# Kernel tuning notes

Hardware: AMD Instinct MI355X
Metric: run time of the kernel (lower is better)

The kernel has to match this reference:

```python
import jax, jax.numpy as jnp
import numpy as np

WIN = 8          # current_window
PRETRAIN = 8     # pretrain_window
HEADS = 8
SHIFT = WIN // 2 # shift_size, shift_dir = [1, 1] (shift_mode=1)
L = WIN * WIN
LOG100 = float(np.log(100.0))


def _shift_mask(H, W):
    # bands (shift_dir=[1,1], no padding). Pairs from different regions get -100.
    hr = np.repeat(np.arange(3), [H - WIN, WIN - SHIFT, SHIFT])
    wr = np.repeat(np.arange(3), [W - WIN, WIN - SHIFT, SHIFT])
    region = hr[:, None] * 3 + wr[None, :]                      # [H, W]
    reg = region.reshape(H // WIN, WIN, W // WIN, WIN)
    reg = reg.transpose(0, 2, 1, 3).reshape(-1, L)              # [nw, L]
    m = np.where(reg[:, :, None] != reg[:, None, :], -100.0, 0.0)
    return jnp.asarray(m, dtype=jnp.float32)[None, :, None]     # [1, nw, 1, L, L]


def _rel_bias(cpb_w1, cpb_b1, cpb_w2):
    # Swin-v2 continuous relative position bias (log-spaced coords + MLP).
    pos = np.stack(np.meshgrid(np.arange(WIN), np.arange(WIN), indexing='ij'), -1).reshape(L, 2)
    rc = (pos[:, None, :] - pos[None, :, :]).astype(np.float32)  # [L, L, 2]
    rc = rc / (PRETRAIN - 1) * 8.0
    rc = np.sign(rc) * np.log2(np.abs(rc) + 1.0) / np.log2(8.0)
    rc = jnp.asarray(rc)
    bias = jax.nn.relu(rc @ cpb_w1 + cpb_b1) @ cpb_w2            # [L, L, heads]
    bias = 16.0 * jax.nn.sigmoid(bias)
    return bias.transpose(2, 0, 1)                               # [heads, L, L]


def _l2n(a):
    # tf.math.l2_normalize with epsilon=1.55e-5
    return a * jax.lax.rsqrt(jnp.maximum(jnp.sum(a * a, -1, keepdims=True), 1.55e-5))


def setup_inputs() -> dict:
    key = jax.random.key(0)
    ks = jax.random.split(key, 6)
    B, H, W, C = 16, 128, 128, 256
    cpb = 512
    return {
        'x': jax.random.normal(ks[0], (B, H, W, C), jnp.float32),
        'qkv_w': jax.random.normal(ks[1], (C, 3 * C), jnp.float32) * 0.02,
        'q_bias': jnp.zeros((C,), jnp.float32),
        'v_bias': jnp.zeros((C,), jnp.float32),
        'scale': jnp.full((HEADS, 1, 1), np.log(10.0), jnp.float32),
        'cpb_w1': jax.random.normal(ks[2], (2, cpb), jnp.float32) * 0.02,
        'cpb_b1': jnp.zeros((cpb,), jnp.float32),
        'cpb_w2': jax.random.normal(ks[3], (cpb, HEADS), jnp.float32) * 0.02,
        'proj_w': jax.random.normal(ks[4], (C, C), jnp.float32) * 0.02,
        'proj_b': jnp.zeros((C,), jnp.float32),
    }


def reference(x, qkv_w, q_bias, v_bias, scale, cpb_w1, cpb_b1, cpb_w2, proj_w, proj_b):
    B, H, W, C = x.shape
    units = C // HEADS
    # qkv 1x1 conv + (q, 0, v) bias
    bias = jnp.concatenate([q_bias, jnp.zeros_like(q_bias), v_bias])
    qkv = jnp.einsum('bhwc,cd->bhwd', x, qkv_w) + bias
    # cyclic shift (H, W > window so shift is applied; no padding needed)
    qkv = jnp.roll(qkv, (-SHIFT, -SHIFT), axis=(1, 2))
    # fused window partition -> [B, nw, heads, L, 3*units]
    nh, nw = H // WIN, W // WIN
    t = qkv.reshape(B, nh, WIN, nw, WIN, HEADS, 3 * units)
    t = t.transpose(0, 1, 3, 5, 2, 4, 6).reshape(B, nh * nw, HEADS, L, 3 * units)
    q, k, v = jnp.split(t, 3, axis=-1)
    # cosine attention with clamped learned logit scale
    logit_scale = jnp.exp(jnp.minimum(scale, LOG100))            # [heads, 1, 1]
    attn = jnp.einsum('bnhld,bnhmd->bnhlm', _l2n(q) * logit_scale, _l2n(k))
    attn = attn + _rel_bias(cpb_w1, cpb_b1, cpb_w2)[None, None] + _shift_mask(H, W)
    attn = jax.nn.softmax(attn, axis=-1)
    out = jnp.einsum('bnhlm,bnhmd->bnhld', attn, v)
    # reverse partition, reverse shift, output projection
    out = out.reshape(B, nh, nw, HEADS, WIN, WIN, units)
    out = out.transpose(0, 1, 4, 2, 5, 3, 6).reshape(B, H, W, C)
    out = jnp.roll(out, (SHIFT, SHIFT), axis=(1, 2))
    return jnp.einsum('bhwc,cd->bhwd', out, proj_w) + proj_b
```

## Files before the change

kernel.cpp:

```cpp
#include <hip/hip_runtime.h>

typedef __attribute__((ext_vector_type(4))) float  f32x4;
typedef __attribute__((ext_vector_type(8))) __bf16 bf16x8;
typedef __attribute__((ext_vector_type(4))) __bf16 bf16x4;

__global__ __launch_bounds__(256) void wprep_kernel(const float* __restrict__ qw,
                                                    const float* __restrict__ pw,
                                                    const float* __restrict__ qb,
                                                    const float* __restrict__ vb,
                                                    __bf16* __restrict__ W2,
                                                    __bf16* __restrict__ Wp,
                                                    float* __restrict__ bcat) {
  int i = blockIdx.x * 256 + threadIdx.x;
  if (i < 24576) {
    int h = i / 3072, rem = i - h * 3072;
    int ft = rem >> 9, rem2 = rem & 511;
    int ks = rem2 >> 6, l = rem2 & 63;
    int g = l >> 4, c = l & 15;
    int col = h * 96 + ft * 16 + c;
    bf16x8 v;
    #pragma unroll
    for (int j = 0; j < 8; ++j)
      v[j] = (__bf16)qw[(ks * 32 + g * 8 + j) * 768 + col];
    *(bf16x8*)(W2 + (size_t)i * 8) = v;
  } else if (i < 24576 + 8192) {
    int j = i - 24576;
    int wv = j >> 10, rem = j & 1023;
    int ft = rem >> 9, rem2 = rem & 511;
    int ks = rem2 >> 6, l = rem2 & 63;
    int g = l >> 4, c = l & 15;
    int col = wv * 32 + ft * 16 + c;
    bf16x8 v;
    #pragma unroll
    for (int j8 = 0; j8 < 8; ++j8)
      v[j8] = (__bf16)pw[(ks * 32 + g * 8 + j8) * 256 + col];
    *(bf16x8*)(Wp + (size_t)j * 8) = v;
  } else if (i < 24576 + 8192 + 768) {
    int cdx = i - 24576 - 8192;
    bcat[cdx] = (cdx < 256) ? qb[cdx] : ((cdx < 512) ? 0.0f : vb[cdx - 512]);
  }
}

__global__ __launch_bounds__(256) void cpb_kernel(const float* __restrict__ w1,
                                                  const float* __restrict__ b1,
                                                  const float* __restrict__ w2,
                                                  float* __restrict__ bias) {
  int pair = blockIdx.x * 256 + threadIdx.x;
  int lq = pair >> 6, mk = pair & 63;
  float d0 = (float)((lq >> 3) - (mk >> 3));
  float d1 = (float)((lq & 7) - (mk & 7));
  float v0 = d0 * (8.0f / 7.0f);
  float v1 = d1 * (8.0f / 7.0f);
  float s0 = (v0 > 0.f) ? 1.f : ((v0 < 0.f) ? -1.f : 0.f);
  float s1 = (v1 > 0.f) ? 1.f : ((v1 < 0.f) ? -1.f : 0.f);
  float r0 = s0 * log2f(fabsf(v0) + 1.0f) * (1.0f / 3.0f);
  float r1 = s1 * log2f(fabsf(v1) + 1.0f) * (1.0f / 3.0f);
  float acc[8] = {0.f, 0.f, 0.f, 0.f, 0.f, 0.f, 0.f, 0.f};
  #pragma unroll 4
  for (int j = 0; j < 512; ++j) {
    float h = fmaxf(r0 * w1[j] + r1 * w1[512 + j] + b1[j], 0.0f);
    #pragma unroll
    for (int q = 0; q < 8; ++q) acc[q] += h * w2[j * 8 + q];
  }
  #pragma unroll
  for (int q = 0; q < 8; ++q) {
    float s = 16.0f / (1.0f + __expf(-acc[q]));
    bias[(q * 64 + lq) * 64 + mk] = s;
  }
}

__device__ __forceinline__ int win_region(int tok, int wi, int wj) {
  int r = tok >> 3, cc = tok & 7;
  int rh = (wi == 15) ? ((r < 4) ? 1 : 2) : 0;
  int rw = (wj == 15) ? ((cc < 4) ? 1 : 2) : 0;
  return rh * 3 + rw;
}

__global__ __launch_bounds__(512, 2) void fused_kernel(
    const float* __restrict__ x, const __bf16* __restrict__ W2,
    const __bf16* __restrict__ Wp, const float* __restrict__ bcat,
    const float* __restrict__ scale, const float* __restrict__ cpb,
    const float* __restrict__ pb, float* __restrict__ outf)
{
  __shared__ __align__(16) __bf16 xs[64 * 256];
  __shared__ __align__(16) __bf16 qkp[8][64 * 72];
  __shared__ __align__(16) __bf16 vst[8][64 * 36];
  const f32x4 zz = {0.f, 0.f, 0.f, 0.f};

  int t = threadIdx.x;
  int h = t >> 6, l = t & 63, g = l >> 4, c = l & 15;
  int win = blockIdx.x, b = blockIdx.y;
  int wi = win >> 4, wj = win & 15;
  bool edge = (wi == 15) || (wj == 15);

  {
    int r = t >> 3;
    int q8 = t & 7;
    int ht = (wi * 8 + (r >> 3) + 4) & 127;
    int wt = (wj * 8 + (r & 7) + 4) & 127;
    const float* src = x + (size_t)((b * 128 + ht) * 128 + wt) * 256 + q8 * 32;
    #pragma unroll
    for (int q = 0; q < 4; ++q) {
      f32x4 a0 = *(const f32x4*)(src + q * 8);
      f32x4 a1 = *(const f32x4*)(src + q * 8 + 4);
      bf16x8 v;
      #pragma unroll
      for (int j = 0; j < 4; ++j) { v[j] = (__bf16)a0[j]; v[4 + j] = (__bf16)a1[j]; }
      int phys = (q8 * 4 + q) ^ (r & 7);
      *(bf16x8*)&xs[r * 256 + phys * 8] = v;
    }
  }
  __syncthreads();

  int toko[4];
  #pragma unroll
  for (int i = 0; i < 4; ++i) {
    int tok = 16 * i + c;
    int ht = (wi * 8 + (tok >> 3) + 4) & 127;
    int wt = (wj * 8 + (tok & 7) + 4) & 127;
    toko[i] = ((b * 128 + ht) * 128 + wt) * 256;
  }

  f32x4 acc[6][4];
  #pragma unroll
  for (int ft = 0; ft < 6; ++ft)
    #pragma unroll
    for (int tt = 0; tt < 4; ++tt) acc[ft][tt] = zz;

  const __bf16* Wh = W2 + (size_t)h * 24576;
  #pragma unroll
  for (int ks = 0; ks < 8; ++ks) {
    bf16x8 wf[6], xf[4];
    #pragma unroll
    for (int ft = 0; ft < 6; ++ft)
      wf[ft] = *(const bf16x8*)(Wh + (size_t)((ft * 8 + ks) * 64 + l) * 8);
    #pragma unroll
    for (int tt = 0; tt < 4; ++tt) {
      int phys = (ks * 4 + g) ^ (c & 7);
      xf[tt] = *(const bf16x8*)&xs[(tt * 16 + c) * 256 + phys * 8];
    }
    #pragma unroll
    for (int ft = 0; ft < 6; ++ft)
      #pragma unroll
      for (int tt = 0; tt < 4; ++tt)
        acc[ft][tt] = __builtin_amdgcn_mfma_f32_16x16x32_bf16(wf[ft], xf[tt], acc[ft][tt], 0, 0, 0);
  }
  __syncthreads();

  #pragma unroll
  for (int ft = 0; ft < 6; ++ft) {
    f32x4 bb = *(const f32x4*)&bcat[h * 96 + ft * 16 + 4 * g];
    #pragma unroll
    for (int tt = 0; tt < 4; ++tt) acc[ft][tt] += bb;
  }

  float ls = __expf(fminf(scale[h], 4.6051701859880914f));

  #pragma unroll
  for (int tt = 0; tt < 4; ++tt) {
    float sq = 0.f, sk = 0.f;
    #pragma unroll
    for (int i = 0; i < 4; ++i) {
      sq += acc[0][tt][i] * acc[0][tt][i] + acc[1][tt][i] * acc[1][tt][i];
      sk += acc[2][tt][i] * acc[2][tt][i] + acc[3][tt][i] * acc[3][tt][i];
    }
    sq += __shfl_xor(sq, 16); sq += __shfl_xor(sq, 32);
    sk += __shfl_xor(sk, 16); sk += __shfl_xor(sk, 32);
    float rq = rsqrtf(fmaxf(sq, 1.55e-5f)) * ls;
    float rk = rsqrtf(fmaxf(sk, 1.55e-5f));
    __bf16* row = &qkp[h][(tt * 16 + c) * 72];
    bf16x4 w0, w1, w2, w3, v0, v1;
    #pragma unroll
    for (int i = 0; i < 4; ++i) {
      w0[i] = (__bf16)(acc[0][tt][i] * rq);
      w1[i] = (__bf16)(acc[1][tt][i] * rq);
      w2[i] = (__bf16)(acc[2][tt][i] * rk);
      w3[i] = (__bf16)(acc[3][tt][i] * rk);
      v0[i] = (__bf16)acc[4][tt][i];
      v1[i] = (__bf16)acc[5][tt][i];
    }
    *(bf16x4*)&row[4 * g]      = w0;
    *(bf16x4*)&row[16 + 4 * g] = w1;
    *(bf16x4*)&row[32 + 4 * g] = w2;
    *(bf16x4*)&row[48 + 4 * g] = w3;
    __bf16* vrow = &vst[h][(tt * 16 + c) * 36];
    *(bf16x4*)&vrow[4 * g]      = v0;
    *(bf16x4*)&vrow[16 + 4 * g] = v1;
  }

  bf16x8 kf[4], qf[4];
  #pragma unroll
  for (int i = 0; i < 4; ++i) {
    kf[i] = *(const bf16x8*)&qkp[h][(16 * i + c) * 72 + 32 + 8 * g];
    qf[i] = *(const bf16x8*)&qkp[h][(16 * i + c) * 72 + 8 * g];
  }

  float rsum[4];
  __bf16* Pw = &qkp[h][0];
  #pragma unroll
  for (int nt = 0; nt < 4; ++nt) {
    f32x4 tt4[4];
    #pragma unroll
    for (int mt = 0; mt < 4; ++mt)
      tt4[mt] = __builtin_amdgcn_mfma_f32_16x16x32_bf16(kf[mt], qf[nt], zz, 0, 0, 0);
    int q = nt * 16 + c;
    float p[16];
    #pragma unroll
    for (int mt = 0; mt < 4; ++mt) {
      f32x4 bb = *(const f32x4*)&cpb[(h * 64 + q) * 64 + mt * 16 + 4 * g];
      #pragma unroll
      for (int i = 0; i < 4; ++i) p[mt * 4 + i] = tt4[mt][i] + bb[i];
    }
    if (edge) {
      int regq = win_region(q, wi, wj);
      #pragma unroll
      for (int mt = 0; mt < 4; ++mt)
        #pragma unroll
        for (int i = 0; i < 4; ++i) {
          int k = mt * 16 + 4 * g + i;
          if (win_region(k, wi, wj) != regq) p[mt * 4 + i] -= 100.0f;
        }
    }
    float mx = -1e30f;
    #pragma unroll
    for (int j = 0; j < 16; ++j) mx = fmaxf(mx, p[j]);
    mx = fmaxf(mx, __shfl_xor(mx, 16));
    mx = fmaxf(mx, __shfl_xor(mx, 32));
    float sum = 0.f;
    #pragma unroll
    for (int j = 0; j < 16; ++j) { p[j] = __expf(p[j] - mx); sum += p[j]; }
    sum += __shfl_xor(sum, 16); sum += __shfl_xor(sum, 32);
    rsum[nt] = sum;
    #pragma unroll
    for (int mt = 0; mt < 4; ++mt) {
      bf16x4 px = { (__bf16)p[mt * 4 + 0], (__bf16)p[mt * 4 + 1],
                    (__bf16)p[mt * 4 + 2], (__bf16)p[mt * 4 + 3] };
      *(bf16x4*)&Pw[q * 72 + mt * 16 + 4 * g] = px;
    }
  }

  #pragma unroll
  for (int mh = 0; mh < 2; ++mh) {
    f32x4 oacc[4];
    #pragma unroll
    for (int nt = 0; nt < 4; ++nt) oacc[nt] = zz;
    #pragma unroll
    for (int ks = 0; ks < 2; ++ks) {
      bf16x8 va;
      #pragma unroll
      for (int j = 0; j < 8; ++j)
        va[j] = vst[h][(32 * ks + 8 * g + j) * 36 + 16 * mh + c];
      #pragma unroll
      for (int nt = 0; nt < 4; ++nt) {
        bf16x8 pfr = *(const bf16x8*)&Pw[(nt * 16 + c) * 72 + 32 * ks + 8 * g];
        oacc[nt] = __builtin_amdgcn_mfma_f32_16x16x32_bf16(va, pfr, oacc[nt], 0, 0, 0);
      }
    }
    int chunk = h * 4 + 2 * mh + (g >> 1);
    #pragma unroll
    for (int nt = 0; nt < 4; ++nt) {
      float rinv = 1.0f / rsum[nt];
      int tok = nt * 16 + c;
      int phys = chunk ^ (tok & 7);
      bf16x4 ov = { (__bf16)(oacc[nt][0] * rinv), (__bf16)(oacc[nt][1] * rinv),
                    (__bf16)(oacc[nt][2] * rinv), (__bf16)(oacc[nt][3] * rinv) };
      *(bf16x4*)&xs[tok * 256 + phys * 8 + 4 * (g & 1)] = ov;
    }
  }
  __syncthreads();

  f32x4 acc2[2][4];
  #pragma unroll
  for (int ft = 0; ft < 2; ++ft)
    #pragma unroll
    for (int tt = 0; tt < 4; ++tt) acc2[ft][tt] = zz;

  const __bf16* Wph = Wp + (size_t)h * 8192;
  #pragma unroll
  for (int ks = 0; ks < 8; ++ks) {
    bf16x8 wf[2], xf[4];
    #pragma unroll
    for (int ft = 0; ft < 2; ++ft)
      wf[ft] = *(const bf16x8*)(Wph + (size_t)((ft * 8 + ks) * 64 + l) * 8);
    #pragma unroll
    for (int tt = 0; tt < 4; ++tt) {
      int phys = (ks * 4 + g) ^ (c & 7);
      xf[tt] = *(const bf16x8*)&xs[(tt * 16 + c) * 256 + phys * 8];
    }
    #pragma unroll
    for (int ft = 0; ft < 2; ++ft)
      #pragma unroll
      for (int tt = 0; tt < 4; ++tt)
        acc2[ft][tt] = __builtin_amdgcn_mfma_f32_16x16x32_bf16(wf[ft], xf[tt], acc2[ft][tt], 0, 0, 0);
  }

  #pragma unroll
  for (int ft = 0; ft < 2; ++ft) {
    f32x4 bb = *(const f32x4*)&pb[h * 32 + ft * 16 + 4 * g];
    #pragma unroll
    for (int tt = 0; tt < 4; ++tt) {
      f32x4 res = acc2[ft][tt] + bb;
      *(f32x4*)&outf[toko[tt] + h * 32 + ft * 16 + 4 * g] = res;
    }
  }
}

extern "C" void kernel_launch(void* const* d_in, const int* in_sizes, int n_in,
                              void* d_out, int out_size, void* d_ws, size_t ws_size,
                              hipStream_t stream)
{
  const float* x      = (const float*)d_in[0];
  const float* qkv_w  = (const float*)d_in[1];
  const float* q_bias = (const float*)d_in[2];
  const float* v_bias = (const float*)d_in[3];
  const float* scale  = (const float*)d_in[4];
  const float* cpb_w1 = (const float*)d_in[5];
  const float* cpb_b1 = (const float*)d_in[6];
  const float* cpb_w2 = (const float*)d_in[7];
  const float* proj_w = (const float*)d_in[8];
  const float* proj_b = (const float*)d_in[9];

  char* ws = (char*)d_ws;
  __bf16* W2   = (__bf16*)(ws);
  __bf16* Wp   = (__bf16*)(ws + 393216LL);
  float*  bcat = (float*) (ws + 524288LL);
  float*  cpb  = (float*) (ws + 527360LL);

  wprep_kernel<<<131, 256, 0, stream>>>(qkv_w, proj_w, q_bias, v_bias, W2, Wp, bcat);
  cpb_kernel<<<16, 256, 0, stream>>>(cpb_w1, cpb_b1, cpb_w2, cpb);
  fused_kernel<<<dim3(256, 16), 512, 0, stream>>>(x, W2, Wp, bcat, scale, cpb,
                                                  proj_b, (float*)d_out);
}
```

Baseline: 430.4 us.

## Keep Q/K/P attention fragments in registers and drop qkp shared buffer

```diff
diff --git a/kernel.cpp b/kernel.cpp
--- a/kernel.cpp
+++ b/kernel.cpp
@@ -76,14 +76,13 @@
   return rh * 3 + rw;
 }
 
-__global__ __launch_bounds__(512, 2) void fused_kernel(
+__global__ __launch_bounds__(512, 4) void fused_kernel(
     const float* __restrict__ x, const __bf16* __restrict__ W2,
     const __bf16* __restrict__ Wp, const float* __restrict__ bcat,
     const float* __restrict__ scale, const float* __restrict__ cpb,
     const float* __restrict__ pb, float* __restrict__ outf)
 {
   __shared__ __align__(16) __bf16 xs[64 * 256];
-  __shared__ __align__(16) __bf16 qkp[8][64 * 72];
   __shared__ __align__(16) __bf16 vst[8][64 * 36];
   const f32x4 zz = {0.f, 0.f, 0.f, 0.f};
 
@@ -156,6 +155,7 @@
 
   float ls = __expf(fminf(scale[h], 4.6051701859880914f));
 
+  bf16x8 kA[4], qB[4];
   #pragma unroll
   for (int tt = 0; tt < 4; ++tt) {
     float sq = 0.f, sk = 0.f;
@@ -168,41 +168,44 @@
     sk += __shfl_xor(sk, 16); sk += __shfl_xor(sk, 32);
     float rq = rsqrtf(fmaxf(sq, 1.55e-5f)) * ls;
     float rk = rsqrtf(fmaxf(sk, 1.55e-5f));
-    __bf16* row = &qkp[h][(tt * 16 + c) * 72];
-    bf16x4 w0, w1, w2, w3, v0, v1;
+    bf16x4 v0, v1;
     #pragma unroll
     for (int i = 0; i < 4; ++i) {
-      w0[i] = (__bf16)(acc[0][tt][i] * rq);
-      w1[i] = (__bf16)(acc[1][tt][i] * rq);
-      w2[i] = (__bf16)(acc[2][tt][i] * rk);
-      w3[i] = (__bf16)(acc[3][tt][i] * rk);
+      qB[tt][i]     = (__bf16)(acc[0][tt][i] * rq);
+      qB[tt][4 + i] = (__bf16)(acc[1][tt][i] * rq);
+      kA[tt][i]     = (__bf16)(acc[2][tt][i] * rk);
+      kA[tt][4 + i] = (__bf16)(acc[3][tt][i] * rk);
       v0[i] = (__bf16)acc[4][tt][i];
       v1[i] = (__bf16)acc[5][tt][i];
     }
-    *(bf16x4*)&row[4 * g]      = w0;
-    *(bf16x4*)&row[16 + 4 * g] = w1;
-    *(bf16x4*)&row[32 + 4 * g] = w2;
-    *(bf16x4*)&row[48 + 4 * g] = w3;
     __bf16* vrow = &vst[h][(tt * 16 + c) * 36];
     *(bf16x4*)&vrow[4 * g]      = v0;
     *(bf16x4*)&vrow[16 + 4 * g] = v1;
   }
 
-  bf16x8 kf[4], qf[4];
-  #pragma unroll
-  for (int i = 0; i < 4; ++i) {
-    kf[i] = *(const bf16x8*)&qkp[h][(16 * i + c) * 72 + 32 + 8 * g];
-    qf[i] = *(const bf16x8*)&qkp[h][(16 * i + c) * 72 + 8 * g];
-  }
-
+  bf16x8 va[2][2];
+  #pragma unroll
+  for (int mh = 0; mh < 2; ++mh)
+    #pragma unroll
+    for (int kp = 0; kp < 2; ++kp)
+      #pragma unroll
+      for (int j = 0; j < 8; ++j)
+        va[mh][kp][j] =
+            vst[h][(32 * kp + 16 * (j >> 2) + 4 * g + (j & 3)) * 36 + 16 * mh + c];
+
+  f32x4 oacc[2][4];
+  #pragma unroll
+  for (int mh = 0; mh < 2; ++mh)
+    #pragma unroll
+    for (int nt = 0; nt < 4; ++nt) oacc[mh][nt] = zz;
   float rsum[4];
-  __bf16* Pw = &qkp[h][0];
+
   #pragma unroll
   for (int nt = 0; nt < 4; ++nt) {
     f32x4 tt4[4];
     #pragma unroll
     for (int mt = 0; mt < 4; ++mt)
-      tt4[mt] = __builtin_amdgcn_mfma_f32_16x16x32_bf16(kf[mt], qf[nt], zz, 0, 0, 0);
+      tt4[mt] = __builtin_amdgcn_mfma_f32_16x16x32_bf16(kA[mt], qB[nt], zz, 0, 0, 0);
     int q = nt * 16 + c;
     float p[16];
     #pragma unroll
@@ -231,39 +234,26 @@
     for (int j = 0; j < 16; ++j) { p[j] = __expf(p[j] - mx); sum += p[j]; }
     sum += __shfl_xor(sum, 16); sum += __shfl_xor(sum, 32);
     rsum[nt] = sum;
-    #pragma unroll
-    for (int mt = 0; mt < 4; ++mt) {
-      bf16x4 px = { (__bf16)p[mt * 4 + 0], (__bf16)p[mt * 4 + 1],
-                    (__bf16)p[mt * 4 + 2], (__bf16)p[mt * 4 + 3] };
-      *(bf16x4*)&Pw[q * 72 + mt * 16 + 4 * g] = px;
+    bf16x8 pf0, pf1;
+    #pragma unroll
+    for (int j = 0; j < 8; ++j) { pf0[j] = (__bf16)p[j]; pf1[j] = (__bf16)p[8 + j]; }
+    #pragma unroll
+    for (int mh = 0; mh < 2; ++mh) {
+      oacc[mh][nt] = __builtin_amdgcn_mfma_f32_16x16x32_bf16(va[mh][0], pf0, oacc[mh][nt], 0, 0, 0);
+      oacc[mh][nt] = __builtin_amdgcn_mfma_f32_16x16x32_bf16(va[mh][1], pf1, oacc[mh][nt], 0, 0, 0);
     }
   }
 
   #pragma unroll
   for (int mh = 0; mh < 2; ++mh) {
-    f32x4 oacc[4];
-    #pragma unroll
-    for (int nt = 0; nt < 4; ++nt) oacc[nt] = zz;
-    #pragma unroll
-    for (int ks = 0; ks < 2; ++ks) {
-      bf16x8 va;
-      #pragma unroll
-      for (int j = 0; j < 8; ++j)
-        va[j] = vst[h][(32 * ks + 8 * g + j) * 36 + 16 * mh + c];
-      #pragma unroll
-      for (int nt = 0; nt < 4; ++nt) {
-        bf16x8 pfr = *(const bf16x8*)&Pw[(nt * 16 + c) * 72 + 32 * ks + 8 * g];
-        oacc[nt] = __builtin_amdgcn_mfma_f32_16x16x32_bf16(va, pfr, oacc[nt], 0, 0, 0);
-      }
-    }
     int chunk = h * 4 + 2 * mh + (g >> 1);
     #pragma unroll
     for (int nt = 0; nt < 4; ++nt) {
       float rinv = 1.0f / rsum[nt];
       int tok = nt * 16 + c;
       int phys = chunk ^ (tok & 7);
-      bf16x4 ov = { (__bf16)(oacc[nt][0] * rinv), (__bf16)(oacc[nt][1] * rinv),
-                    (__bf16)(oacc[nt][2] * rinv), (__bf16)(oacc[nt][3] * rinv) };
+      bf16x4 ov = { (__bf16)(oacc[mh][nt][0] * rinv), (__bf16)(oacc[mh][nt][1] * rinv),
+                    (__bf16)(oacc[mh][nt][2] * rinv), (__bf16)(oacc[mh][nt][3] * rinv) };
       *(bf16x4*)&xs[tok * 256 + phys * 8 + 4 * (g & 1)] = ov;
     }
   }
```

Result: slower. 722.2 us (+67.8%).

## Split output projection into separate kernel via bf16 intermediate; merge prep kernels

Applied to the files above, without the earlier changes.

```diff
diff --git a/kernel.cpp b/kernel.cpp
--- a/kernel.cpp
+++ b/kernel.cpp
@@ -4,68 +4,66 @@
 typedef __attribute__((ext_vector_type(8))) __bf16 bf16x8;
 typedef __attribute__((ext_vector_type(4))) __bf16 bf16x4;
 
-__global__ __launch_bounds__(256) void wprep_kernel(const float* __restrict__ qw,
-                                                    const float* __restrict__ pw,
-                                                    const float* __restrict__ qb,
-                                                    const float* __restrict__ vb,
-                                                    __bf16* __restrict__ W2,
-                                                    __bf16* __restrict__ Wp,
-                                                    float* __restrict__ bcat) {
-  int i = blockIdx.x * 256 + threadIdx.x;
-  if (i < 24576) {
-    int h = i / 3072, rem = i - h * 3072;
-    int ft = rem >> 9, rem2 = rem & 511;
-    int ks = rem2 >> 6, l = rem2 & 63;
-    int g = l >> 4, c = l & 15;
-    int col = h * 96 + ft * 16 + c;
-    bf16x8 v;
-    #pragma unroll
-    for (int j = 0; j < 8; ++j)
-      v[j] = (__bf16)qw[(ks * 32 + g * 8 + j) * 768 + col];
-    *(bf16x8*)(W2 + (size_t)i * 8) = v;
-  } else if (i < 24576 + 8192) {
-    int j = i - 24576;
-    int wv = j >> 10, rem = j & 1023;
-    int ft = rem >> 9, rem2 = rem & 511;
-    int ks = rem2 >> 6, l = rem2 & 63;
-    int g = l >> 4, c = l & 15;
-    int col = wv * 32 + ft * 16 + c;
-    bf16x8 v;
-    #pragma unroll
-    for (int j8 = 0; j8 < 8; ++j8)
-      v[j8] = (__bf16)pw[(ks * 32 + g * 8 + j8) * 256 + col];
-    *(bf16x8*)(Wp + (size_t)j * 8) = v;
-  } else if (i < 24576 + 8192 + 768) {
-    int cdx = i - 24576 - 8192;
-    bcat[cdx] = (cdx < 256) ? qb[cdx] : ((cdx < 512) ? 0.0f : vb[cdx - 512]);
-  }
-}
-
-__global__ __launch_bounds__(256) void cpb_kernel(const float* __restrict__ w1,
-                                                  const float* __restrict__ b1,
-                                                  const float* __restrict__ w2,
-                                                  float* __restrict__ bias) {
-  int pair = blockIdx.x * 256 + threadIdx.x;
-  int lq = pair >> 6, mk = pair & 63;
-  float d0 = (float)((lq >> 3) - (mk >> 3));
-  float d1 = (float)((lq & 7) - (mk & 7));
-  float v0 = d0 * (8.0f / 7.0f);
-  float v1 = d1 * (8.0f / 7.0f);
-  float s0 = (v0 > 0.f) ? 1.f : ((v0 < 0.f) ? -1.f : 0.f);
-  float s1 = (v1 > 0.f) ? 1.f : ((v1 < 0.f) ? -1.f : 0.f);
-  float r0 = s0 * log2f(fabsf(v0) + 1.0f) * (1.0f / 3.0f);
-  float r1 = s1 * log2f(fabsf(v1) + 1.0f) * (1.0f / 3.0f);
-  float acc[8] = {0.f, 0.f, 0.f, 0.f, 0.f, 0.f, 0.f, 0.f};
-  #pragma unroll 4
-  for (int j = 0; j < 512; ++j) {
-    float h = fmaxf(r0 * w1[j] + r1 * w1[512 + j] + b1[j], 0.0f);
-    #pragma unroll
-    for (int q = 0; q < 8; ++q) acc[q] += h * w2[j * 8 + q];
-  }
-  #pragma unroll
-  for (int q = 0; q < 8; ++q) {
-    float s = 16.0f / (1.0f + __expf(-acc[q]));
-    bias[(q * 64 + lq) * 64 + mk] = s;
+__global__ __launch_bounds__(256) void prep_kernel(
+    const float* __restrict__ qw, const float* __restrict__ pw,
+    const float* __restrict__ qb, const float* __restrict__ vb,
+    const float* __restrict__ w1, const float* __restrict__ b1,
+    const float* __restrict__ w2,
+    __bf16* __restrict__ W2, __bf16* __restrict__ Wp,
+    float* __restrict__ bcat, float* __restrict__ cpbias)
+{
+  if (blockIdx.x < 131) {
+    int i = blockIdx.x * 256 + threadIdx.x;
+    if (i < 24576) {
+      int h = i / 3072, rem = i - h * 3072;
+      int ft = rem >> 9, rem2 = rem & 511;
+      int ks = rem2 >> 6, l = rem2 & 63;
+      int g = l >> 4, c = l & 15;
+      int col = h * 96 + ft * 16 + c;
+      bf16x8 v;
+      #pragma unroll
+      for (int j = 0; j < 8; ++j)
+        v[j] = (__bf16)qw[(ks * 32 + g * 8 + j) * 768 + col];
+      *(bf16x8*)(W2 + (size_t)i * 8) = v;
+    } else if (i < 24576 + 8192) {
+      int j = i - 24576;
+      int wv = j >> 10, rem = j & 1023;
+      int ft = rem >> 9, rem2 = rem & 511;
+      int ks = rem2 >> 6, l = rem2 & 63;
+      int g = l >> 4, c = l & 15;
+      int col = wv * 32 + ft * 16 + c;
+      bf16x8 v;
+      #pragma unroll
+      for (int j8 = 0; j8 < 8; ++j8)
+        v[j8] = (__bf16)pw[(ks * 32 + g * 8 + j8) * 256 + col];
+      *(bf16x8*)(Wp + (size_t)j * 8) = v;
+    } else if (i < 24576 + 8192 + 768) {
+      int cdx = i - 24576 - 8192;
+      bcat[cdx] = (cdx < 256) ? qb[cdx] : ((cdx < 512) ? 0.0f : vb[cdx - 512]);
+    }
+  } else {
+    int pair = (blockIdx.x - 131) * 256 + threadIdx.x;
+    int lq = pair >> 6, mk = pair & 63;
+    float d0 = (float)((lq >> 3) - (mk >> 3));
+    float d1 = (float)((lq & 7) - (mk & 7));
+    float v0 = d0 * (8.0f / 7.0f);
+    float v1 = d1 * (8.0f / 7.0f);
+    float s0 = (v0 > 0.f) ? 1.f : ((v0 < 0.f) ? -1.f : 0.f);
+    float s1 = (v1 > 0.f) ? 1.f : ((v1 < 0.f) ? -1.f : 0.f);
+    float r0 = s0 * log2f(fabsf(v0) + 1.0f) * (1.0f / 3.0f);
+    float r1 = s1 * log2f(fabsf(v1) + 1.0f) * (1.0f / 3.0f);
+    float acc[8] = {0.f, 0.f, 0.f, 0.f, 0.f, 0.f, 0.f, 0.f};
+    #pragma unroll 4
+    for (int j = 0; j < 512; ++j) {
+      float h = fmaxf(r0 * w1[j] + r1 * w1[512 + j] + b1[j], 0.0f);
+      #pragma unroll
+      for (int q = 0; q < 8; ++q) acc[q] += h * w2[j * 8 + q];
+    }
+    #pragma unroll
+    for (int q = 0; q < 8; ++q) {
+      float s = 16.0f / (1.0f + __expf(-acc[q]));
+      cpbias[(q * 64 + lq) * 64 + mk] = s;
+    }
   }
 }
 
@@ -78,9 +76,8 @@
 
 __global__ __launch_bounds__(512, 2) void fused_kernel(
     const float* __restrict__ x, const __bf16* __restrict__ W2,
-    const __bf16* __restrict__ Wp, const float* __restrict__ bcat,
-    const float* __restrict__ scale, const float* __restrict__ cpb,
-    const float* __restrict__ pb, float* __restrict__ outf)
+    const float* __restrict__ bcat, const float* __restrict__ scale,
+    const float* __restrict__ cpb, __bf16* __restrict__ out)
 {
   __shared__ __align__(16) __bf16 xs[64 * 256];
   __shared__ __align__(16) __bf16 qkp[8][64 * 72];
@@ -145,7 +142,6 @@
       for (int tt = 0; tt < 4; ++tt)
         acc[ft][tt] = __builtin_amdgcn_mfma_f32_16x16x32_bf16(wf[ft], xf[tt], acc[ft][tt], 0, 0, 0);
   }
-  __syncthreads();
 
   #pragma unroll
   for (int ft = 0; ft < 6; ++ft) {
@@ -256,51 +252,66 @@
         oacc[nt] = __builtin_amdgcn_mfma_f32_16x16x32_bf16(va, pfr, oacc[nt], 0, 0, 0);
       }
     }
-    int chunk = h * 4 + 2 * mh + (g >> 1);
     #pragma unroll
     for (int nt = 0; nt < 4; ++nt) {
       float rinv = 1.0f / rsum[nt];
-      int tok = nt * 16 + c;
-      int phys = chunk ^ (tok & 7);
       bf16x4 ov = { (__bf16)(oacc[nt][0] * rinv), (__bf16)(oacc[nt][1] * rinv),
                     (__bf16)(oacc[nt][2] * rinv), (__bf16)(oacc[nt][3] * rinv) };
-      *(bf16x4*)&xs[tok * 256 + phys * 8 + 4 * (g & 1)] = ov;
+      *(bf16x4*)(out + toko[nt] + h * 32 + 16 * mh + 4 * g) = ov;
+    }
+  }
+}
+
+__global__ __launch_bounds__(512, 4) void proj2_kernel(
+    const __bf16* __restrict__ A, const __bf16* __restrict__ Wp,
+    const float* __restrict__ pb, float* __restrict__ outf)
+{
+  __shared__ __align__(16) __bf16 os[128 * 256];
+  const f32x4 zz = {0.f, 0.f, 0.f, 0.f};
+  int t = threadIdx.x;
+  int wv = t >> 6, l = t & 63, g = l >> 4, c = l & 15;
+  int mblk = blockIdx.x;
+
+  {
+    int r = t >> 2;
+    int q4 = t & 3;
+    const __bf16* src = A + (size_t)(mblk * 128 + r) * 256 + q4 * 64;
+    #pragma unroll
+    for (int q = 0; q < 8; ++q) {
+      bf16x8 v = *(const bf16x8*)(src + q * 8);
+      int phys = (q4 * 8 + q) ^ (r & 7);
+      *(bf16x8*)&os[r * 256 + phys * 8] = v;
     }
   }
   __syncthreads();
 
-  f32x4 acc2[2][4];
+  f32x4 acc[2][8];
   #pragma unroll
   for (int ft = 0; ft < 2; ++ft)
     #pragma unroll
-    for (int tt = 0; tt < 4; ++tt) acc2[ft][tt] = zz;
-
-  const __bf16* Wph = Wp + (size_t)h * 8192;
+    for (int tt = 0; tt < 8; ++tt) acc[ft][tt] = zz;
+
+  const __bf16* Wph = Wp + (size_t)wv * 8192;
   #pragma unroll
   for (int ks = 0; ks < 8; ++ks) {
-    bf16x8 wf[2], xf[4];
-    #pragma unroll
-    for (int ft = 0; ft < 2; ++ft)
-      wf[ft] = *(const bf16x8*)(Wph + (size_t)((ft * 8 + ks) * 64 + l) * 8);
-    #pragma unroll
-    for (int tt = 0; tt < 4; ++tt) {
+    bf16x8 w0 = *(const bf16x8*)(Wph + (size_t)((0 * 8 + ks) * 64 + l) * 8);
+    bf16x8 w1 = *(const bf16x8*)(Wph + (size_t)((1 * 8 + ks) * 64 + l) * 8);
+    #pragma unroll
+    for (int tt = 0; tt < 8; ++tt) {
       int phys = (ks * 4 + g) ^ (c & 7);
-      xf[tt] = *(const bf16x8*)&xs[(tt * 16 + c) * 256 + phys * 8];
-    }
-    #pragma unroll
-    for (int ft = 0; ft < 2; ++ft)
-      #pragma unroll
-      for (int tt = 0; tt < 4; ++tt)
-        acc2[ft][tt] = __builtin_amdgcn_mfma_f32_16x16x32_bf16(wf[ft], xf[tt], acc2[ft][tt], 0, 0, 0);
+      bf16x8 xf = *(const bf16x8*)&os[(tt * 16 + c) * 256 + phys * 8];
+      acc[0][tt] = __builtin_amdgcn_mfma_f32_16x16x32_bf16(w0, xf, acc[0][tt], 0, 0, 0);
+      acc[1][tt] = __builtin_amdgcn_mfma_f32_16x16x32_bf16(w1, xf, acc[1][tt], 0, 0, 0);
+    }
   }
 
   #pragma unroll
   for (int ft = 0; ft < 2; ++ft) {
-    f32x4 bb = *(const f32x4*)&pb[h * 32 + ft * 16 + 4 * g];
-    #pragma unroll
-    for (int tt = 0; tt < 4; ++tt) {
-      f32x4 res = acc2[ft][tt] + bb;
-      *(f32x4*)&outf[toko[tt] + h * 32 + ft * 16 + 4 * g] = res;
+    f32x4 bb = *(const f32x4*)&pb[wv * 32 + ft * 16 + 4 * g];
+    #pragma unroll
+    for (int tt = 0; tt < 8; ++tt) {
+      f32x4 res = acc[ft][tt] + bb;
+      *(f32x4*)&outf[(size_t)(mblk * 128 + tt * 16 + c) * 256 + wv * 32 + ft * 16 + 4 * g] = res;
     }
   }
 }
@@ -321,13 +332,14 @@
   const float* proj_b = (const float*)d_in[9];
 
   char* ws = (char*)d_ws;
-  __bf16* W2   = (__bf16*)(ws);
-  __bf16* Wp   = (__bf16*)(ws + 393216LL);
-  float*  bcat = (float*) (ws + 524288LL);
-  float*  cpb  = (float*) (ws + 527360LL);
-
-  wprep_kernel<<<131, 256, 0, stream>>>(qkv_w, proj_w, q_bias, v_bias, W2, Wp, bcat);
-  cpb_kernel<<<16, 256, 0, stream>>>(cpb_w1, cpb_b1, cpb_w2, cpb);
-  fused_kernel<<<dim3(256, 16), 512, 0, stream>>>(x, W2, Wp, bcat, scale, cpb,
-                                                  proj_b, (float*)d_out);
-}
+  __bf16* aout = (__bf16*)(ws);
+  __bf16* W2   = (__bf16*)(ws + 134217728LL);
+  __bf16* Wp   = (__bf16*)(ws + 134610944LL);
+  float*  bcat = (float*) (ws + 134742016LL);
+  float*  cpb  = (float*) (ws + 134745088LL);
+
+  prep_kernel<<<147, 256, 0, stream>>>(qkv_w, proj_w, q_bias, v_bias,
+                                       cpb_w1, cpb_b1, cpb_w2, W2, Wp, bcat, cpb);
+  fused_kernel<<<dim3(256, 16), 512, 0, stream>>>(x, W2, bcat, scale, cpb, aout);
+  proj2_kernel<<<2048, 512, 0, stream>>>(aout, Wp, proj_b, (float*)d_out);
+}
```

New measurement: 399.9 us. 7.1% less time.
